# Optimization experiments

Hardware: AMD Instinct MI355X
Metric: run time of the kernel (lower is better)

## Reference

```python
import jax, jax.numpy as jnp
import numpy as np

COMMITMENT_COST = 0.25


def setup_inputs() -> dict:
    key = jax.random.key(0)
    k1, k2 = jax.random.split(key)
    inputs = jax.random.normal(k1, (8, 1024, 512), dtype=jnp.float32)
    codebook = jax.random.normal(k2, (8192, 512), dtype=jnp.float32)
    return {"inputs": inputs, "codebook": codebook}


def reference(inputs, codebook):
    B, S, D = inputs.shape
    flat = inputs.reshape(-1, D)  # [N, D]
    distances = (
        jnp.sum(flat * flat, axis=1, keepdims=True)
        + jnp.sum(codebook * codebook, axis=1)
        - 2.0 * flat @ codebook.T
    )
    encoding_indices = jnp.argmin(distances, axis=1)  # [N] int
    min_distances = jnp.min(distances, axis=1)  # [N]
    quantized = codebook[encoding_indices].reshape(inputs.shape)  # [B,S,D]
    # straight-through estimator
    quantized_st = inputs + jax.lax.stop_gradient(quantized - inputs)
    # mse losses with reduction='sum'; .detach() -> stop_gradient
    loss_vq = jnp.sum((quantized - jax.lax.stop_gradient(inputs)) ** 2)
    loss_commit = jnp.sum((inputs - jax.lax.stop_gradient(quantized)) ** 2)
    # non-EMA branch: loss = commitment_cost * loss_commit + loss_vq
    loss = loss_commit * COMMITMENT_COST + loss_vq
    return (
        quantized_st,
        loss,
        encoding_indices.reshape(B, S),
        min_distances.reshape(B, S),
        loss_commit,
    )
```

## Files before the change

### kernel.cpp

```cpp
#include <hip/hip_runtime.h>

typedef __attribute__((ext_vector_type(8)))  short short8;
typedef __attribute__((ext_vector_type(16))) float f32x16;
typedef unsigned short ushort_t;
typedef unsigned int uint32;

#define NROWS 8192
#define NCODE 8192
#define DIM   512

#define OUT_Q      0
#define OUT_LOSS   4194304
#define OUT_IDX    4194305
#define OUT_MIND   4202497
#define OUT_COMMIT 4210689

#define WS_ENORM  0
#define WS_PMIN   8192
#define WS_PIDX   73728
#define WS_LPART  147456
#define WS_BHI    150528
#define WS_BLO    2247680

__device__ inline uint32 bf16_rne(float f) {
    uint32 u = __float_as_uint(f);
    return (u + 0x7FFFu + ((u >> 16) & 1u)) >> 16;
}

__device__ inline void gload16(const ushort_t* g, ushort_t* l) {
    __builtin_amdgcn_global_load_lds(
        (const __attribute__((address_space(1))) void*)g,
        (__attribute__((address_space(3))) void*)l, 16, 0, 0);
}

__global__ __launch_bounds__(256) void conv_kernel(const float* __restrict__ x,
                                                   const float* __restrict__ cb,
                                                   ushort_t* __restrict__ ahi,
                                                   ushort_t* __restrict__ alo,
                                                   ushort_t* __restrict__ bhi,
                                                   ushort_t* __restrict__ blo,
                                                   float* __restrict__ enorm) {
    int gid  = blockIdx.x * 256 + threadIdx.x;
    bool isA = gid < 524288;
    int g    = isA ? gid : gid - 524288;
    int row  = g >> 6;
    int lane = g & 63;
    int k0   = lane * 8;
    const float* src = (isA ? x : cb) + (size_t)row * DIM + k0;
    float v[8];
    *(float4*)&v[0] = *(const float4*)src;
    *(float4*)&v[4] = *(const float4*)(src + 4);
    float s = 0.0f;
    uint32 h[8], l[8];
    #pragma unroll
    for (int i = 0; i < 8; ++i) {
        s += v[i] * v[i];
        h[i] = bf16_rne(v[i]);
        float hf = __uint_as_float(h[i] << 16);
        l[i] = bf16_rne(v[i] - hf);
    }
    int tile = (row >> 7) * 16 + (k0 >> 5);
    int rp = row & 127, kp = k0 & 31;
    int c  = (rp >> 5) * 2 + (kp >> 4);
    int L  = (rp & 31) + (((kp >> 3) & 1) << 5);
    size_t off = (size_t)tile * 4096 + c * 512 + L * 8;
    uint4 ph, pl;
    ph.x = h[0] | (h[1] << 16); ph.y = h[2] | (h[3] << 16);
    ph.z = h[4] | (h[5] << 16); ph.w = h[6] | (h[7] << 16);
    pl.x = l[0] | (l[1] << 16); pl.y = l[2] | (l[3] << 16);
    pl.z = l[4] | (l[5] << 16); pl.w = l[6] | (l[7] << 16);
    if (isA) {
        *(uint4*)(ahi + off) = ph;
        *(uint4*)(alo + off) = pl;
    } else {
        *(uint4*)(bhi + off) = ph;
        *(uint4*)(blo + off) = pl;
        #pragma unroll
        for (int o = 32; o > 0; o >>= 1) s += __shfl_down(s, o);
        if (lane == 0) enorm[row] = s;
    }
}

__global__ __launch_bounds__(256, 2) void vq_mfma_kernel(
        const ushort_t* __restrict__ ahi, const ushort_t* __restrict__ alo,
        const ushort_t* __restrict__ bhi, const ushort_t* __restrict__ blo,
        const float* __restrict__ enorm,
        float* __restrict__ pmin, int* __restrict__ pidx) {
    __shared__ __align__(16) ushort_t smem[32768];

    const int tid  = threadIdx.x;
    const int wave = tid >> 6, lane = tid & 63;
    const int l31  = lane & 31, half = lane >> 5;
    const int q  = blockIdx.x;
    const int bx = (q & 7) * 8 + (q >> 6);
    const int by = (q >> 3) & 7;
    const int wrow = (wave >> 1) * 64;
    const int wcol = (wave & 1) * 64;
    const int so = wave * 512 + lane * 8;

    f32x16 acc[2][2];
    #pragma unroll
    for (int i = 0; i < 2; ++i)
        #pragma unroll
        for (int j = 0; j < 2; ++j)
            #pragma unroll
            for (int r = 0; r < 16; ++r) acc[i][j][r] = 0.0f;

    float bestd[32];
    int   besti[32];
    #pragma unroll
    for (int i = 0; i < 32; ++i) { bestd[i] = 3.4e38f; besti[i] = 0x7FFFFFFF; }

    auto stage = [&](int n) {
        const int kb = n & 15;
        const int ctile = by * 8 + (n >> 4);
        const size_t at = (size_t)(bx * 16 + kb) * 4096;
        const size_t bt = (size_t)(ctile * 16 + kb) * 4096;
        ushort_t* S = smem + (n & 1) * 16384;
        gload16(ahi + at + so,        S + so);
        gload16(ahi + at + 2048 + so, S + 2048 + so);
        gload16(alo + at + so,        S + 4096 + so);
        gload16(alo + at + 2048 + so, S + 6144 + so);
        gload16(bhi + bt + so,        S + 8192 + so);
        gload16(bhi + bt + 2048 + so, S + 10240 + so);
        gload16(blo + bt + so,        S + 12288 + so);
        gload16(blo + bt + 2048 + so, S + 14336 + so);
    };

    stage(0);

    for (int n = 0; n < 128; ++n) {
        __syncthreads();
        if (n + 1 < 128) stage(n + 1);

        ushort_t* S = smem + (n & 1) * 16384;
        #pragma unroll
        for (int k16 = 0; k16 < 2; ++k16) {
            short8 ah[2], al[2], bh[2], bl[2];
            #pragma unroll
            for (int ti = 0; ti < 2; ++ti) {
                int ca = ((wrow >> 5) + ti) * 2 + k16;
                ah[ti] = *(const short8*)&S[ca * 512 + lane * 8];
                al[ti] = *(const short8*)&S[4096 + ca * 512 + lane * 8];
            }
            #pragma unroll
            for (int tj = 0; tj < 2; ++tj) {
                int cb_ = ((wcol >> 5) + tj) * 2 + k16;
                bh[tj] = *(const short8*)&S[8192 + cb_ * 512 + lane * 8];
                bl[tj] = *(const short8*)&S[12288 + cb_ * 512 + lane * 8];
            }
            #pragma unroll
            for (int ti = 0; ti < 2; ++ti)
                #pragma unroll
                for (int tj = 0; tj < 2; ++tj) {
                    acc[ti][tj] = __builtin_amdgcn_mfma_f32_32x32x16_bf16(
                        ah[ti], bh[tj], acc[ti][tj], 0, 0, 0);
                    acc[ti][tj] = __builtin_amdgcn_mfma_f32_32x32x16_bf16(
                        ah[ti], bl[tj], acc[ti][tj], 0, 0, 0);
                    acc[ti][tj] = __builtin_amdgcn_mfma_f32_32x32x16_bf16(
                        al[ti], bh[tj], acc[ti][tj], 0, 0, 0);
                }
        }

        if ((n & 15) == 15) {
            const int ct = n >> 4;
            const int colbase = by * 1024 + ct * 128 + wcol;
            #pragma unroll
            for (int tj = 0; tj < 2; ++tj) {
                const int ci = colbase + tj * 32 + l31;
                const float en = enorm[ci];
                #pragma unroll
                for (int ti = 0; ti < 2; ++ti)
                    #pragma unroll
                    for (int reg = 0; reg < 16; ++reg) {
                        float d = en - 2.0f * acc[ti][tj][reg];
                        int s = ti * 16 + reg;
                        if (d < bestd[s]) { bestd[s] = d; besti[s] = ci; }
                    }
            }
            #pragma unroll
            for (int i = 0; i < 2; ++i)
                #pragma unroll
                for (int j = 0; j < 2; ++j)
                    #pragma unroll
                    for (int r = 0; r < 16; ++r) acc[i][j][r] = 0.0f;
        }
    }

    float* rd = (float*)smem;
    int*   ri = (int*)smem + 8192;
    __syncthreads();
    const int slot = (wave & 1) * 32 + l31;
    #pragma unroll
    for (int ti = 0; ti < 2; ++ti)
        #pragma unroll
        for (int reg = 0; reg < 16; ++reg) {
            int row = wrow + ti * 32 + (reg & 3) + 8 * (reg >> 2) + 4 * half;
            rd[slot * 128 + row] = bestd[ti * 16 + reg];
            ri[slot * 128 + row] = besti[ti * 16 + reg];
        }
    __syncthreads();
    if (tid < 128) {
        float bd = rd[tid];
        int   bi = ri[tid];
        #pragma unroll 8
        for (int t = 1; t < 64; ++t) {
            float d = rd[t * 128 + tid];
            int  ii = ri[t * 128 + tid];
            if (d < bd || (d == bd && ii < bi)) { bd = d; bi = ii; }
        }
        pmin[(size_t)(bx * 128 + tid) * 8 + by] = bd;
        pidx[(size_t)(bx * 128 + tid) * 8 + by] = bi;
    }
}

__global__ __launch_bounds__(256) void finish_kernel(const float* __restrict__ x,
                                                     const float* __restrict__ cb,
                                                     const float* __restrict__ pmin,
                                                     const int* __restrict__ pidx,
                                                     float* __restrict__ out_idx,
                                                     float* __restrict__ qout,
                                                     float* __restrict__ out_mind,
                                                     float* __restrict__ lpart) {
    __shared__ float sred[4];
    int row  = blockIdx.x * 4 + (threadIdx.x >> 6);
    int lane = threadIdx.x & 63;

    float d = (lane < 8) ? pmin[(size_t)row * 8 + lane] : 3.4e38f;
    int  ii = (lane < 8) ? pidx[(size_t)row * 8 + lane] : 0x7FFFFFFF;
    #pragma unroll
    for (int o = 4; o > 0; o >>= 1) {
        float d2 = __shfl_down(d, o);
        int   i2 = __shfl_down(ii, o);
        if (d2 < d || (d2 == d && i2 < ii)) { d = d2; ii = i2; }
    }
    int idx = __shfl(ii, 0);
    if (lane == 0) out_idx[row] = (float)idx;

    const float4* e4 = (const float4*)(cb + (size_t)idx * DIM);
    const float4* x4 = (const float4*)(x + (size_t)row * DIM);
    float4* q4 = (float4*)(qout + (size_t)row * DIM);
    float s = 0.0f;
    #pragma unroll
    for (int u = 0; u < 2; ++u) {
        float4 e  = e4[lane + u * 64];
        float4 xv = x4[lane + u * 64];
        q4[lane + u * 64] = e;
        float dx = xv.x - e.x, dy = xv.y - e.y, dz = xv.z - e.z, dw = xv.w - e.w;
        s += dx * dx + dy * dy + dz * dz + dw * dw;
    }
    #pragma unroll
    for (int o = 32; o > 0; o >>= 1) s += __shfl_down(s, o);
    if (lane == 0) { sred[threadIdx.x >> 6] = s; out_mind[row] = s; }
    __syncthreads();
    if (threadIdx.x == 0) lpart[blockIdx.x] = sred[0] + sred[1] + sred[2] + sred[3];
}

__global__ __launch_bounds__(256) void loss_kernel(const float* __restrict__ lpart,
                                                   float* __restrict__ out_loss,
                                                   float* __restrict__ out_commit) {
    __shared__ float sm[256];
    float s = 0.0f;
    for (int i = threadIdx.x; i < 2048; i += 256) s += lpart[i];
    sm[threadIdx.x] = s;
    __syncthreads();
    #pragma unroll
    for (int o = 128; o > 0; o >>= 1) {
        if (threadIdx.x < o) sm[threadIdx.x] += sm[threadIdx.x + o];
        __syncthreads();
    }
    if (threadIdx.x == 0) {
        *out_commit = sm[0];
        *out_loss   = 1.25f * sm[0];
    }
}

extern "C" void kernel_launch(void* const* d_in, const int* in_sizes, int n_in,
                              void* d_out, int out_size, void* d_ws, size_t ws_size,
                              hipStream_t stream) {
    const float* x  = (const float*)d_in[0];
    const float* cb = (const float*)d_in[1];
    float* out = (float*)d_out;
    float* ws  = (float*)d_ws;

    ushort_t* ahi = (ushort_t*)d_out;
    ushort_t* alo = (ushort_t*)d_out + 4194304;
    ushort_t* bhi = (ushort_t*)(ws + WS_BHI);
    ushort_t* blo = (ushort_t*)(ws + WS_BLO);
    float* enorm = ws + WS_ENORM;
    float* pmin  = ws + WS_PMIN;
    int*   pidx  = (int*)(ws + WS_PIDX);
    float* lpart = ws + WS_LPART;

    conv_kernel<<<4096, 256, 0, stream>>>(x, cb, ahi, alo, bhi, blo, enorm);
    vq_mfma_kernel<<<512, 256, 0, stream>>>(ahi, alo, bhi, blo, enorm, pmin, pidx);
    finish_kernel<<<NROWS / 4, 256, 0, stream>>>(x, cb, pmin, pidx,
                                                 out + OUT_IDX, out + OUT_Q,
                                                 out + OUT_MIND, lpart);
    loss_kernel<<<1, 256, 0, stream>>>(lpart, out + OUT_LOSS, out + OUT_COMMIT);
}
```

Baseline: 278.4 us.

## Load MFMA operands directly from global into registers, dropping LDS staging

Replaces the double-buffered global-to-LDS staging and its per-iteration barriers with per-wave direct global loads into registers, double-buffered in two register sets across k16 phases. It removes LDS traffic and __syncthreads, relying on the pre-tiled layout and L2 for reuse. Each wave now fetches its own A and B fragments, so operands shared between waves are no longer shared in LDS, global/L2 traffic grows, and more VGPRs are used.

```diff
diff --git a/kernel.cpp b/kernel.cpp
--- a/kernel.cpp
+++ b/kernel.cpp
@@ -25,12 +25,6 @@
 __device__ inline uint32 bf16_rne(float f) {
     uint32 u = __float_as_uint(f);
     return (u + 0x7FFFu + ((u >> 16) & 1u)) >> 16;
-}
-
-__device__ inline void gload16(const ushort_t* g, ushort_t* l) {
-    __builtin_amdgcn_global_load_lds(
-        (const __attribute__((address_space(1))) void*)g,
-        (__attribute__((address_space(3))) void*)l, 16, 0, 0);
 }
 
 __global__ __launch_bounds__(256) void conv_kernel(const float* __restrict__ x,
@@ -96,7 +90,8 @@
     const int by = (q >> 3) & 7;
     const int wrow = (wave >> 1) * 64;
     const int wcol = (wave & 1) * 64;
-    const int so = wave * 512 + lane * 8;
+    const int aoff = (wrow >> 6) * 2048 + lane * 8;
+    const int boff = (wcol >> 6) * 2048 + lane * 8;
 
     f32x16 acc[2][2];
     #pragma unroll
@@ -111,59 +106,50 @@
     #pragma unroll
     for (int i = 0; i < 32; ++i) { bestd[i] = 3.4e38f; besti[i] = 0x7FFFFFFF; }
 
-    auto stage = [&](int n) {
-        const int kb = n & 15;
-        const int ctile = by * 8 + (n >> 4);
-        const size_t at = (size_t)(bx * 16 + kb) * 4096;
-        const size_t bt = (size_t)(ctile * 16 + kb) * 4096;
-        ushort_t* S = smem + (n & 1) * 16384;
-        gload16(ahi + at + so,        S + so);
-        gload16(ahi + at + 2048 + so, S + 2048 + so);
-        gload16(alo + at + so,        S + 4096 + so);
-        gload16(alo + at + 2048 + so, S + 6144 + so);
-        gload16(bhi + bt + so,        S + 8192 + so);
-        gload16(bhi + bt + 2048 + so, S + 10240 + so);
-        gload16(blo + bt + so,        S + 12288 + so);
-        gload16(blo + bt + 2048 + so, S + 14336 + so);
+    auto loadPhase = [&](int p, short8* P) {
+        const int n = p >> 1, k16 = p & 1;
+        const size_t abase = (size_t)(bx * 16 + (n & 15)) * 4096;
+        const size_t bbase = (size_t)(by * 128 + n) * 4096;
+        const ushort_t* pa = ahi + abase + aoff;
+        const ushort_t* qa = alo + abase + aoff;
+        const ushort_t* pb = bhi + bbase + boff;
+        const ushort_t* qb = blo + bbase + boff;
+        P[0] = *(const short8*)(pa + (k16) * 512);
+        P[1] = *(const short8*)(pa + (2 + k16) * 512);
+        P[2] = *(const short8*)(qa + (k16) * 512);
+        P[3] = *(const short8*)(qa + (2 + k16) * 512);
+        P[4] = *(const short8*)(pb + (k16) * 512);
+        P[5] = *(const short8*)(pb + (2 + k16) * 512);
+        P[6] = *(const short8*)(qb + (k16) * 512);
+        P[7] = *(const short8*)(qb + (2 + k16) * 512);
     };
 
-    stage(0);
-
-    for (int n = 0; n < 128; ++n) {
-        __syncthreads();
-        if (n + 1 < 128) stage(n + 1);
-
-        ushort_t* S = smem + (n & 1) * 16384;
-        #pragma unroll
-        for (int k16 = 0; k16 < 2; ++k16) {
-            short8 ah[2], al[2], bh[2], bl[2];
-            #pragma unroll
-            for (int ti = 0; ti < 2; ++ti) {
-                int ca = ((wrow >> 5) + ti) * 2 + k16;
-                ah[ti] = *(const short8*)&S[ca * 512 + lane * 8];
-                al[ti] = *(const short8*)&S[4096 + ca * 512 + lane * 8];
+    auto computePhase = [&](const short8* P) {
+        #pragma unroll
+        for (int ti = 0; ti < 2; ++ti)
+            #pragma unroll
+            for (int tj = 0; tj < 2; ++tj) {
+                acc[ti][tj] = __builtin_amdgcn_mfma_f32_32x32x16_bf16(
+                    P[ti], P[4 + tj], acc[ti][tj], 0, 0, 0);
+                acc[ti][tj] = __builtin_amdgcn_mfma_f32_32x32x16_bf16(
+                    P[ti], P[6 + tj], acc[ti][tj], 0, 0, 0);
+                acc[ti][tj] = __builtin_amdgcn_mfma_f32_32x32x16_bf16(
+                    P[2 + ti], P[4 + tj], acc[ti][tj], 0, 0, 0);
             }
-            #pragma unroll
-            for (int tj = 0; tj < 2; ++tj) {
-                int cb_ = ((wcol >> 5) + tj) * 2 + k16;
-                bh[tj] = *(const short8*)&S[8192 + cb_ * 512 + lane * 8];
-                bl[tj] = *(const short8*)&S[12288 + cb_ * 512 + lane * 8];
-            }
-            #pragma unroll
-            for (int ti = 0; ti < 2; ++ti)
-                #pragma unroll
-                for (int tj = 0; tj < 2; ++tj) {
-                    acc[ti][tj] = __builtin_amdgcn_mfma_f32_32x32x16_bf16(
-                        ah[ti], bh[tj], acc[ti][tj], 0, 0, 0);
-                    acc[ti][tj] = __builtin_amdgcn_mfma_f32_32x32x16_bf16(
-                        ah[ti], bl[tj], acc[ti][tj], 0, 0, 0);
-                    acc[ti][tj] = __builtin_amdgcn_mfma_f32_32x32x16_bf16(
-                        al[ti], bh[tj], acc[ti][tj], 0, 0, 0);
-                }
-        }
-
-        if ((n & 15) == 15) {
-            const int ct = n >> 4;
+    };
+
+    short8 P0[8], P1[8];
+    loadPhase(0, P0);
+    loadPhase(1, P1);
+
+    for (int p = 0; p < 256; p += 2) {
+        computePhase(P0);
+        if (p + 2 < 256) loadPhase(p + 2, P0);
+        computePhase(P1);
+        if (p + 3 < 256) loadPhase(p + 3, P1);
+
+        if ((p & 31) == 30) {
+            const int ct = p >> 5;
             const int colbase = by * 1024 + ct * 128 + wcol;
             #pragma unroll
             for (int tj = 0; tj < 2; ++tj) {
```

After: 302.0 us. 1.08x slower.
